# Optimization experiments

Measured on AMD Instinct MI355X. Metric: run time of the kernel, lower is better.

## Reference

```python
import jax, jax.numpy as jnp
import numpy as np

TEACHER_BOX = (-0.9, 0.9, -0.9, 0.9)  # x1, x2, y1, y2
STUDENT_BOX = (-0.8, 0.8, -0.8, 0.8)
STUDENT_TEMP = 0.1
TEACHER_TEMP = 0.04


def _box_grids(t_box, s_box, H, W):
    # Faithful to DINOLoss.box_to_grid: grid size derives from the TEACHER box,
    # meshgrid stacked as (y, x) -- torch quirk replicated (grid_sample reads ch0 as x).
    x1, x2, y1, y2 = t_box
    gW = int(abs(x1 - x2) / 2 * W)
    gH = int(abs(y1 - y2) / 2 * H)
    ty, tx = jnp.linspace(y1, y2, gH), jnp.linspace(x1, x2, gW)
    tgrid = jnp.stack(jnp.meshgrid(ty, tx, indexing='ij'), axis=-1)  # [gH, gW, 2]
    x1, x2, y1, y2 = s_box
    sy, sx = jnp.linspace(y1, y2, gH), jnp.linspace(x1, x2, gW)
    sgrid = jnp.stack(jnp.meshgrid(sy, sx, indexing='ij'), axis=-1)  # [gH, gW, 2]
    return tgrid, sgrid


def grid_sample_border(feat, grid):
    # feat: [B, C, H, W]; grid: [gh, gw, 2]; torch convention: grid[...,0]->x, grid[...,1]->y
    # bilinear, align_corners=False, padding_mode='border'
    B, C, H, W = feat.shape
    gx, gy = grid[..., 0], grid[..., 1]
    ix = jnp.clip(((gx + 1.0) * W - 1.0) * 0.5, 0.0, W - 1.0)
    iy = jnp.clip(((gy + 1.0) * H - 1.0) * 0.5, 0.0, H - 1.0)
    ix0 = jnp.floor(ix).astype(jnp.int32)
    iy0 = jnp.floor(iy).astype(jnp.int32)
    ix1 = jnp.clip(ix0 + 1, 0, W - 1)
    iy1 = jnp.clip(iy0 + 1, 0, H - 1)
    ix0 = jnp.clip(ix0, 0, W - 1)
    iy0 = jnp.clip(iy0, 0, H - 1)
    wx = ix - ix0
    wy = iy - iy0
    v00 = feat[:, :, iy0, ix0]  # [B, C, gh, gw]
    v01 = feat[:, :, iy0, ix1]
    v10 = feat[:, :, iy1, ix0]
    v11 = feat[:, :, iy1, ix1]
    return (v00 * (1 - wy) * (1 - wx) + v01 * (1 - wy) * wx
            + v10 * wy * (1 - wx) + v11 * wy * wx)


def setup_inputs() -> dict:
    key = jax.random.key(0)
    k1, k2, k3 = jax.random.split(key, 3)
    teacher_feat = jax.random.normal(k1, (8, 8192, 28, 28), dtype=jnp.float32)
    student_feat = jax.random.normal(k2, (8, 8192, 12, 12), dtype=jnp.float32)
    center = jax.random.normal(k3, (1, 8192), dtype=jnp.float32)
    return {"teacher_feat": teacher_feat, "student_feat": student_feat, "center": center}


def reference(teacher_feat, student_feat, center):
    H, W = teacher_feat.shape[-2:]
    tgrid, sgrid = _box_grids(TEACHER_BOX, STUDENT_BOX, H, W)
    # teacher: centered + sharpened softmax over channel dim (detached in original)
    t_prob = jax.nn.softmax((teacher_feat - center[:, :, None, None]) / TEACHER_TEMP, axis=1)
    t_common = jax.lax.stop_gradient(grid_sample_border(t_prob, tgrid))  # [B, C, gh, gw]
    s_common = grid_sample_border(student_feat / STUDENT_TEMP, sgrid)    # [B, C, gh, gw]
    loss = (-t_common * jax.nn.log_softmax(s_common, axis=1)).sum(axis=1).mean()
    return loss
```

## Files before the change

kernel.cpp:

```cpp
#include <hip/hip_runtime.h>
#include <hip/hip_bf16.h>

typedef __attribute__((ext_vector_type(8))) short  short8;
typedef __attribute__((ext_vector_type(4))) float  float4v;
typedef __attribute__((ext_vector_type(4))) unsigned short ushort4v;

#define NC    8192
#define TPIX  784
#define NB    8

#define WS_M2    0
#define WS_O     250880
#define WS_ZACC  283648
#define WS_DACC  308736
#define WS_ZPOS  333824
#define WS_ZERO_OFF WS_ZACC
#define WS_ZERO_LEN 70176
#define WS_STUDB 360448
#define WS_NEED  (360448 + 65536*320)

__device__ __forceinline__ unsigned short bf16rne(float f) {
    unsigned int u = __float_as_uint(f);
    u = (u + 0x7FFFu + ((u >> 16) & 1u)) >> 16;
    return (unsigned short)u;
}

__device__ __forceinline__ short8 cvt8(float4v a, float4v b) {
    union { __hip_bfloat162 h[4]; short8 s; } u;
    u.h[0] = __float22bfloat162_rn(float2{a[0], a[1]});
    u.h[1] = __float22bfloat162_rn(float2{a[2], a[3]});
    u.h[2] = __float22bfloat162_rn(float2{b[0], b[1]});
    u.h[3] = __float22bfloat162_rn(float2{b[2], b[3]});
    return u.s;
}

__global__ void k_init_m2(unsigned short* __restrict__ m2) {
    int p  = blockIdx.x;
    int sp = threadIdx.x;
    int y = p / 28, x = p % 28;
    float val = 0.f;
    if (sp < 144) {
        int v = sp / 12, u = sp % 12;
        float kyv = 0.f, kxu = 0.f;
        for (int a = 0; a < 25; ++a) {
            float ctc = 0.9f + 1.05f * (float)a;
            int   i0  = (int)ctc; float wt = ctc - (float)i0;
            float Ay  = (i0 == y) ? (1.f - wt) : ((i0 + 1 == y) ? wt : 0.f);
            float Ax  = (i0 == x) ? (1.f - wt) : ((i0 + 1 == x) ? wt : 0.f);
            float csc = 0.7f + 0.4f * (float)a;
            int   j0  = (int)csc; float wsv = csc - (float)j0;
            float Bv  = (j0 == v) ? (1.f - wsv) : ((j0 + 1 == v) ? wsv : 0.f);
            float Bu  = (j0 == u) ? (1.f - wsv) : ((j0 + 1 == u) ? wsv : 0.f);
            kyv += Ay * Bv;
            kxu += Ax * Bu;
        }
        val = 10.f * kyv * kxu;
    }
    m2[p * 160 + sp] = bf16rne(val);
}

__launch_bounds__(256)
__global__ void k_pre(const float* __restrict__ student, const float* __restrict__ center,
                      unsigned short* __restrict__ studb, float* __restrict__ o) {
    const int tid = blockIdx.x * 256 + threadIdx.x;
    const int row = tid / 20, ch = tid % 20;
    short8 hv = {0,0,0,0,0,0,0,0};
    if (ch < 18) {
        const float* src = student + (long long)row * 144 + ch * 8;
        hv = cvt8(*(const float4v*)(src), *(const float4v*)(src + 4));
    }
    *(short8*)(studb + (long long)row * 160 + ch * 8) = hv;
    if (ch == 0 && row < NC)
        o[row] = fmaf(36.0673762f, center[row], 233.7165966f);
}

template<bool PRE>
__launch_bounds__(256, 2)
__global__ void k_main(const float* __restrict__ teacher,
                       const float* __restrict__ student,
                       const float* __restrict__ center,
                       const unsigned short* __restrict__ m2,
                       const unsigned short* __restrict__ studb,
                       const float* __restrict__ o,
                       float* __restrict__ zacc, float* __restrict__ dacc) {
    const int b  = blockIdx.z;
    const int cg = blockIdx.y;
    const int t  = threadIdx.x;
    const int w = t >> 6, lane = t & 63, l15 = lane & 15, g = lane >> 4;

    const int tile0 = (blockIdx.x * 4 + w) * 2;
    const bool va = (tile0     < 49);
    const bool vb = (tile0 + 1 < 49);
    const int p0a = va ? tile0 * 16 : 0;
    const int p0b = vb ? (tile0 + 1) * 16 : 0;

    short8 afa[5], afb[5];
    {
        const unsigned short* ra = m2 + (p0a + l15) * 160;
        const unsigned short* rb = m2 + (p0b + l15) * 160;
        #pragma unroll
        for (int ks = 0; ks < 5; ++ks) {
            afa[ks] = *(const short8*)(ra + ks * 32 + g * 8);
            afb[ks] = *(const short8*)(rb + ks * 32 + g * 8);
        }
    }

    float sEa[4] = {0.f,0.f,0.f,0.f}, sEYa[4] = {0.f,0.f,0.f,0.f};
    float sEb[4] = {0.f,0.f,0.f,0.f}, sEYb[4] = {0.f,0.f,0.f,0.f};

    const long long tbase = (long long)(b * NC) * TPIX;
    const long long sbase = (long long)(b * NC) * 144;
    const short8 zfrag = {0,0,0,0,0,0,0,0};

    for (int cc = 0; cc < 8; ++cc) {
        const int cA = cg * 256 + cc * 32 + l15;
        const int cB = cA + 16;

        short8 bfA[5], bfB[5];
        float oA, oB;
        if (PRE) {
            const unsigned short* rA = studb + ((long long)(b * NC) + cA) * 160;
            const unsigned short* rB = rA + 16 * 160;
            #pragma unroll
            for (int ks = 0; ks < 5; ++ks) {
                bfA[ks] = *(const short8*)(rA + ks * 32 + g * 8);
                bfB[ks] = *(const short8*)(rB + ks * 32 + g * 8);
            }
            oA = o[cA];
            oB = o[cB];
        } else {
            const float* sA = student + sbase + (long long)cA * 144;
            const float* sB = sA + 16 * 144;
            #pragma unroll
            for (int ks = 0; ks < 4; ++ks) {
                bfA[ks] = cvt8(*(const float4v*)(sA + ks * 32 + g * 8),
                               *(const float4v*)(sA + ks * 32 + g * 8 + 4));
                bfB[ks] = cvt8(*(const float4v*)(sB + ks * 32 + g * 8),
                               *(const float4v*)(sB + ks * 32 + g * 8 + 4));
            }
            bfA[4] = (g < 2) ? cvt8(*(const float4v*)(sA + 128 + g * 8),
                                    *(const float4v*)(sA + 128 + g * 8 + 4)) : zfrag;
            bfB[4] = (g < 2) ? cvt8(*(const float4v*)(sB + 128 + g * 8),
                                    *(const float4v*)(sB + 128 + g * 8 + 4)) : zfrag;
            oA = fmaf(36.0673762f, center[cA], 233.7165966f);
            oB = fmaf(36.0673762f, center[cB], 233.7165966f);
        }

        const float* trA = teacher + tbase + (long long)cA * TPIX;
        const float* trB = trA + 16LL * TPIX;
        float4v tvAa = *(const float4v*)(trA + p0a + 4 * g);
        float4v tvAb = *(const float4v*)(trA + p0b + 4 * g);
        float4v tvBa = *(const float4v*)(trB + p0a + 4 * g);
        float4v tvBb = *(const float4v*)(trB + p0b + 4 * g);

        float4v accAa = {0.f,0.f,0.f,0.f}, accAb = {0.f,0.f,0.f,0.f};
        float4v accBa = {0.f,0.f,0.f,0.f}, accBb = {0.f,0.f,0.f,0.f};
        #pragma unroll
        for (int ks = 0; ks < 5; ++ks) {
            accAa = __builtin_amdgcn_mfma_f32_16x16x32_bf16(afa[ks], bfA[ks], accAa, 0, 0, 0);
            accAb = __builtin_amdgcn_mfma_f32_16x16x32_bf16(afb[ks], bfA[ks], accAb, 0, 0, 0);
            accBa = __builtin_amdgcn_mfma_f32_16x16x32_bf16(afa[ks], bfB[ks], accBa, 0, 0, 0);
            accBb = __builtin_amdgcn_mfma_f32_16x16x32_bf16(afb[ks], bfB[ks], accBb, 0, 0, 0);
        }

        #pragma unroll
        for (int i = 0; i < 4; ++i) {
            float e0 = exp2f(fmaf(36.0673762f, tvAa[i], -oA));
            sEa[i] += e0;  sEYa[i] = fmaf(e0, accAa[i], sEYa[i]);
            float e1 = exp2f(fmaf(36.0673762f, tvAb[i], -oA));
            sEb[i] += e1;  sEYb[i] = fmaf(e1, accAb[i], sEYb[i]);
            float e2 = exp2f(fmaf(36.0673762f, tvBa[i], -oB));
            sEa[i] += e2;  sEYa[i] = fmaf(e2, accBa[i], sEYa[i]);
            float e3 = exp2f(fmaf(36.0673762f, tvBb[i], -oB));
            sEb[i] += e3;  sEYb[i] = fmaf(e3, accBb[i], sEYb[i]);
        }
    }

    #pragma unroll
    for (int i = 0; i < 4; ++i) {
        float e0 = sEa[i], y0 = sEYa[i], e1 = sEb[i], y1 = sEYb[i];
        e0 += __shfl_xor(e0, 1); e0 += __shfl_xor(e0, 2); e0 += __shfl_xor(e0, 4); e0 += __shfl_xor(e0, 8);
        y0 += __shfl_xor(y0, 1); y0 += __shfl_xor(y0, 2); y0 += __shfl_xor(y0, 4); y0 += __shfl_xor(y0, 8);
        e1 += __shfl_xor(e1, 1); e1 += __shfl_xor(e1, 2); e1 += __shfl_xor(e1, 4); e1 += __shfl_xor(e1, 8);
        y1 += __shfl_xor(y1, 1); y1 += __shfl_xor(y1, 2); y1 += __shfl_xor(y1, 4); y1 += __shfl_xor(y1, 8);
        if (l15 == 0) {
            if (va) {
                atomicAdd(zacc + b * TPIX + p0a + 4 * g + i, e0);
                atomicAdd(dacc + b * TPIX + p0a + 4 * g + i, y0);
            }
            if (vb) {
                atomicAdd(zacc + b * TPIX + p0b + 4 * g + i, e1);
                atomicAdd(dacc + b * TPIX + p0b + 4 * g + i, y1);
            }
        }
    }
}

__launch_bounds__(256)
__global__ void k_lse(const float* __restrict__ student, float* __restrict__ zpos) {
    const int cg = blockIdx.x;
    const int a  = blockIdx.y;
    const int b  = blockIdx.z;
    const int t  = threadIdx.x;

    const float cv = 0.7f + 0.4f * (float)a;
    const int   v0 = (int)cv;
    const float wv = cv - (float)v0;
    const float W0 = 10.f * (1.f - wv), W1 = 10.f * wv;

    float accs[25];
    #pragma unroll
    for (int p = 0; p < 25; ++p) accs[p] = 0.f;

    for (int j = 0; j < 8; ++j) {
        const int c = cg * 2048 + 256 * j + t;
        const float* row = student + (long long)(b * NC + c) * 144 + v0 * 12;
        float4v r0 = *(const float4v*)(row + 0);
        float4v r1 = *(const float4v*)(row + 4);
        float4v r2 = *(const float4v*)(row + 8);
        float4v s0 = *(const float4v*)(row + 12);
        float4v s1 = *(const float4v*)(row + 16);
        float4v s2 = *(const float4v*)(row + 20);

        float R[12];
        #pragma unroll
        for (int u = 0; u < 4; ++u) {
            R[u]     = fmaf(W0, r0[u], W1 * s0[u]);
            R[u + 4] = fmaf(W0, r1[u], W1 * s1[u]);
            R[u + 8] = fmaf(W0, r2[u], W1 * s2[u]);
        }
        #pragma unroll
        for (int p = 0; p < 25; ++p) {
            const float cu = 0.7f + 0.4f * (float)p;
            const int   u0 = (int)cu;
            const float wu = cu - (float)u0;
            float sc = fmaf(1.f - wu, R[u0], wu * R[u0 + 1]);
            accs[p] += exp2f(fmaf(1.44269504f, sc, -86.5617025f));
        }
    }

    #pragma unroll
    for (int p = 0; p < 25; ++p) {
        float v = accs[p];
        #pragma unroll
        for (int m = 1; m < 64; m <<= 1) v += __shfl_xor(v, m);
        accs[p] = v;
    }
    if ((t & 63) == 0) {
        #pragma unroll
        for (int p = 0; p < 25; ++p)
            atomicAdd(zpos + (b * 25 + a) * 25 + p, accs[p]);
    }
}

__global__ void k_final(const float* __restrict__ zacc, const float* __restrict__ dacc,
                        const float* __restrict__ zpos, float* __restrict__ out) {
    __shared__ float red[8];
    int t = threadIdx.x;
    float s = 0.f;
    for (int i = t; i < 5000; i += 256) s += 60.f + logf(zpos[i]);
    for (int i = t; i < NB * TPIX; i += 256) s -= dacc[i] / zacc[i];
    for (int m = 1; m < 64; m <<= 1) s += __shfl_xor(s, m);
    if ((t & 63) == 0) red[t >> 6] = s;
    __syncthreads();
    if (t == 0) out[0] = (red[0] + red[1] + red[2] + red[3]) * (1.f / 5000.f);
}

extern "C" void kernel_launch(void* const* d_in, const int* in_sizes, int n_in,
                              void* d_out, int out_size, void* d_ws, size_t ws_size,
                              hipStream_t stream) {
    const float* teacher = (const float*)d_in[0];
    const float* student = (const float*)d_in[1];
    const float* center  = (const float*)d_in[2];

    char* ws = (char*)d_ws;
    unsigned short* m2    = (unsigned short*)(ws + WS_M2);
    float*          oarr  = (float*)(ws + WS_O);
    float*          zacc  = (float*)(ws + WS_ZACC);
    float*          dacc  = (float*)(ws + WS_DACC);
    float*          zpos  = (float*)(ws + WS_ZPOS);
    unsigned short* studb = (unsigned short*)(ws + WS_STUDB);

    hipMemsetAsync(ws + WS_ZERO_OFF, 0, WS_ZERO_LEN, stream);
    k_init_m2<<<784, 160, 0, stream>>>(m2);

    if (ws_size >= (size_t)WS_NEED) {
        k_pre<<<5120, 256, 0, stream>>>(student, center, studb, oarr);
        k_main<true><<<dim3(7, 32, 8), 256, 0, stream>>>(teacher, student, center, m2,
                                                         studb, oarr, zacc, dacc);
    } else {
        k_main<false><<<dim3(7, 32, 8), 256, 0, stream>>>(teacher, student, center, m2,
                                                          studb, oarr, zacc, dacc);
    }
    k_lse<<<dim3(4, 25, 8), 256, 0, stream>>>(student, zpos);
    k_final<<<1, 256, 0, stream>>>(zacc, dacc, zpos, (float*)d_out);
}
```

Measured before the change: 156.0 us.

## Stage interpolation matrix in LDS and tile six pixel tiles per wave

Adds a new main kernel that copies a 96-row slab of the bf16 interpolation matrix into shared memory. Each wave then walks its channels across six 16-pixel tiles, so every student fragment loaded from global memory is reused across six MFMA tiles instead of two. The grid shifts from many small blocks to 9x8x8 blocks of 512 threads, with 24 accumulator pairs per thread. This raises register pressure, adds LDS reads, and leaves some tiles idle in the last pixel group. The fallback kernel is simplified to process one channel group per iteration.

```diff
diff --git a/kernel.cpp b/kernel.cpp
--- a/kernel.cpp
+++ b/kernel.cpp
@@ -74,15 +74,93 @@
         o[row] = fmaf(36.0673762f, center[row], 233.7165966f);
 }
 
-template<bool PRE>
+__launch_bounds__(512, 4)
+__global__ void k_main2(const float* __restrict__ teacher,
+                        const unsigned short* __restrict__ m2,
+                        const unsigned short* __restrict__ studb,
+                        const float* __restrict__ o,
+                        float* __restrict__ zacc, float* __restrict__ dacc) {
+    __shared__ unsigned short m2s[96 * 168];
+
+    const int b  = blockIdx.z;
+    const int cw = blockIdx.y;
+    const int pg = blockIdx.x;
+    const int t  = threadIdx.x;
+    const int w = t >> 6, lane = t & 63, l15 = lane & 15, g = lane >> 4;
+
+    for (int i = t; i < 3840; i += 512) {
+        const int r = i / 40, c4 = i % 40;
+        const int rg = pg * 96 + r;
+        ushort4v v = {0, 0, 0, 0};
+        if (rg < TPIX) v = *(const ushort4v*)(m2 + rg * 160 + c4 * 4);
+        *(ushort4v*)&m2s[r * 168 + c4 * 4] = v;
+    }
+    __syncthreads();
+
+    float sE[24], sEY[24];
+    #pragma unroll
+    for (int j = 0; j < 24; ++j) { sE[j] = 0.f; sEY[j] = 0.f; }
+
+    const long long tbase = (long long)(b * NC) * TPIX;
+
+    for (int k = 0; k < 8; ++k) {
+        const int c = cw * 1024 + k * 128 + w * 16 + l15;
+
+        const unsigned short* srow = studb + ((long long)(b * NC) + c) * 160;
+        short8 bf[5];
+        #pragma unroll
+        for (int ks = 0; ks < 5; ++ks)
+            bf[ks] = *(const short8*)(srow + ks * 32 + g * 8);
+        const float oc = o[c];
+
+        const float* trow = teacher + tbase + (long long)c * TPIX;
+
+        #pragma unroll
+        for (int t6 = 0; t6 < 6; ++t6) {
+            if (pg * 6 + t6 > 48) continue;
+            const int p0 = pg * 96 + t6 * 16;
+
+            float4v tv = *(const float4v*)(trow + p0 + 4 * g);
+
+            float4v acc = {0.f, 0.f, 0.f, 0.f};
+            #pragma unroll
+            for (int ks = 0; ks < 5; ++ks) {
+                short8 af = *(const short8*)&m2s[(t6 * 16 + l15) * 168 + ks * 32 + g * 8];
+                acc = __builtin_amdgcn_mfma_f32_16x16x32_bf16(af, bf[ks], acc, 0, 0, 0);
+            }
+
+            #pragma unroll
+            for (int i = 0; i < 4; ++i) {
+                float e = exp2f(fmaf(36.0673762f, tv[i], -oc));
+                sE[t6 * 4 + i] += e;
+                sEY[t6 * 4 + i] = fmaf(e, acc[i], sEY[t6 * 4 + i]);
+            }
+        }
+    }
+
+    #pragma unroll
+    for (int t6 = 0; t6 < 6; ++t6) {
+        if (pg * 6 + t6 > 48) continue;
+        #pragma unroll
+        for (int i = 0; i < 4; ++i) {
+            float e = sE[t6 * 4 + i], y = sEY[t6 * 4 + i];
+            e += __shfl_xor(e, 1); e += __shfl_xor(e, 2); e += __shfl_xor(e, 4); e += __shfl_xor(e, 8);
+            y += __shfl_xor(y, 1); y += __shfl_xor(y, 2); y += __shfl_xor(y, 4); y += __shfl_xor(y, 8);
+            if (l15 == 0) {
+                const int p = pg * 96 + t6 * 16 + 4 * g + i;
+                atomicAdd(zacc + b * TPIX + p, e);
+                atomicAdd(dacc + b * TPIX + p, y);
+            }
+        }
+    }
+}
+
 __launch_bounds__(256, 2)
-__global__ void k_main(const float* __restrict__ teacher,
-                       const float* __restrict__ student,
-                       const float* __restrict__ center,
-                       const unsigned short* __restrict__ m2,
-                       const unsigned short* __restrict__ studb,
-                       const float* __restrict__ o,
-                       float* __restrict__ zacc, float* __restrict__ dacc) {
+__global__ void k_main_fb(const float* __restrict__ teacher,
+                          const float* __restrict__ student,
+                          const float* __restrict__ center,
+                          const unsigned short* __restrict__ m2,
+                          float* __restrict__ zacc, float* __restrict__ dacc) {
     const int b  = blockIdx.z;
     const int cg = blockIdx.y;
     const int t  = threadIdx.x;
@@ -107,72 +185,36 @@
 
     float sEa[4] = {0.f,0.f,0.f,0.f}, sEYa[4] = {0.f,0.f,0.f,0.f};
     float sEb[4] = {0.f,0.f,0.f,0.f}, sEYb[4] = {0.f,0.f,0.f,0.f};
-
     const long long tbase = (long long)(b * NC) * TPIX;
     const long long sbase = (long long)(b * NC) * 144;
     const short8 zfrag = {0,0,0,0,0,0,0,0};
 
-    for (int cc = 0; cc < 8; ++cc) {
-        const int cA = cg * 256 + cc * 32 + l15;
-        const int cB = cA + 16;
-
-        short8 bfA[5], bfB[5];
-        float oA, oB;
-        if (PRE) {
-            const unsigned short* rA = studb + ((long long)(b * NC) + cA) * 160;
-            const unsigned short* rB = rA + 16 * 160;
-            #pragma unroll
-            for (int ks = 0; ks < 5; ++ks) {
-                bfA[ks] = *(const short8*)(rA + ks * 32 + g * 8);
-                bfB[ks] = *(const short8*)(rB + ks * 32 + g * 8);
-            }
-            oA = o[cA];
-            oB = o[cB];
-        } else {
-            const float* sA = student + sbase + (long long)cA * 144;
-            const float* sB = sA + 16 * 144;
-            #pragma unroll
-            for (int ks = 0; ks < 4; ++ks) {
-                bfA[ks] = cvt8(*(const float4v*)(sA + ks * 32 + g * 8),
-                               *(const float4v*)(sA + ks * 32 + g * 8 + 4));
-                bfB[ks] = cvt8(*(const float4v*)(sB + ks * 32 + g * 8),
-                               *(const float4v*)(sB + ks * 32 + g * 8 + 4));
-            }
-            bfA[4] = (g < 2) ? cvt8(*(const float4v*)(sA + 128 + g * 8),
-                                    *(const float4v*)(sA + 128 + g * 8 + 4)) : zfrag;
-            bfB[4] = (g < 2) ? cvt8(*(const float4v*)(sB + 128 + g * 8),
-                                    *(const float4v*)(sB + 128 + g * 8 + 4)) : zfrag;
-            oA = fmaf(36.0673762f, center[cA], 233.7165966f);
-            oB = fmaf(36.0673762f, center[cB], 233.7165966f);
-        }
-
+    for (int cc = 0; cc < 16; ++cc) {
+        const int cA = cg * 256 + cc * 16 + l15;
+        const float* sA = student + sbase + (long long)cA * 144;
+        short8 bfA[5];
+        #pragma unroll
+        for (int ks = 0; ks < 4; ++ks)
+            bfA[ks] = cvt8(*(const float4v*)(sA + ks * 32 + g * 8),
+                           *(const float4v*)(sA + ks * 32 + g * 8 + 4));
+        bfA[4] = (g < 2) ? cvt8(*(const float4v*)(sA + 128 + g * 8),
+                                *(const float4v*)(sA + 128 + g * 8 + 4)) : zfrag;
+        const float oA = fmaf(36.0673762f, center[cA], 233.7165966f);
         const float* trA = teacher + tbase + (long long)cA * TPIX;
-        const float* trB = trA + 16LL * TPIX;
-        float4v tvAa = *(const float4v*)(trA + p0a + 4 * g);
-        float4v tvAb = *(const float4v*)(trA + p0b + 4 * g);
-        float4v tvBa = *(const float4v*)(trB + p0a + 4 * g);
-        float4v tvBb = *(const float4v*)(trB + p0b + 4 * g);
-
-        float4v accAa = {0.f,0.f,0.f,0.f}, accAb = {0.f,0.f,0.f,0.f};
-        float4v accBa = {0.f,0.f,0.f,0.f}, accBb = {0.f,0.f,0.f,0.f};
+        float4v tva = *(const float4v*)(trA + p0a + 4 * g);
+        float4v tvb = *(const float4v*)(trA + p0b + 4 * g);
+        float4v acca = {0.f,0.f,0.f,0.f}, accb = {0.f,0.f,0.f,0.f};
         #pragma unroll
         for (int ks = 0; ks < 5; ++ks) {
-            accAa = __builtin_amdgcn_mfma_f32_16x16x32_bf16(afa[ks], bfA[ks], accAa, 0, 0, 0);
-            accAb = __builtin_amdgcn_mfma_f32_16x16x32_bf16(afb[ks], bfA[ks], accAb, 0, 0, 0);
-            accBa = __builtin_amdgcn_mfma_f32_16x16x32_bf16(afa[ks], bfB[ks], accBa, 0, 0, 0);
-            accBb = __builtin_amdgcn_mfma_f32_16x16x32_bf16(afb[ks], bfB[ks], accBb, 0, 0, 0);
-        }
-
+            acca = __builtin_amdgcn_mfma_f32_16x16x32_bf16(afa[ks], bfA[ks], acca, 0, 0, 0);
+            accb = __builtin_amdgcn_mfma_f32_16x16x32_bf16(afb[ks], bfA[ks], accb, 0, 0, 0);
+        }
         #pragma unroll
         for (int i = 0; i < 4; ++i) {
-            float e0 = exp2f(fmaf(36.0673762f, tvAa[i], -oA));
-            sEa[i] += e0;  sEYa[i] = fmaf(e0, accAa[i], sEYa[i]);
-            float e1 = exp2f(fmaf(36.0673762f, tvAb[i], -oA));
-            sEb[i] += e1;  sEYb[i] = fmaf(e1, accAb[i], sEYb[i]);
-            float e2 = exp2f(fmaf(36.0673762f, tvBa[i], -oB));
-            sEa[i] += e2;  sEYa[i] = fmaf(e2, accBa[i], sEYa[i]);
-            float e3 = exp2f(fmaf(36.0673762f, tvBb[i], -oB));
-            sEb[i] += e3;  sEYb[i] = fmaf(e3, accBb[i], sEYb[i]);
+            float e0 = exp2f(fmaf(36.0673762f, tva[i], -oA));
+            sEa[i] += e0;  sEYa[i] = fmaf(e0, acca[i], sEYa[i]);
+            float e1 = exp2f(fmaf(36.0673762f, tvb[i], -oA));
+            sEb[i] += e1;  sEYb[i] = fmaf(e1, accb[i], sEYb[i]);
         }
     }
 
@@ -286,11 +328,9 @@
 
     if (ws_size >= (size_t)WS_NEED) {
         k_pre<<<5120, 256, 0, stream>>>(student, center, studb, oarr);
-        k_main<true><<<dim3(7, 32, 8), 256, 0, stream>>>(teacher, student, center, m2,
-                                                         studb, oarr, zacc, dacc);
+        k_main2<<<dim3(9, 8, 8), 512, 0, stream>>>(teacher, m2, studb, oarr, zacc, dacc);
     } else {
-        k_main<false><<<dim3(7, 32, 8), 256, 0, stream>>>(teacher, student, center, m2,
-                                                          studb, oarr, zacc, dacc);
+        k_main_fb<<<dim3(7, 32, 8), 256, 0, stream>>>(teacher, student, center, m2, zacc, dacc);
     }
     k_lse<<<dim3(4, 25, 8), 256, 0, stream>>>(student, zpos);
     k_final<<<1, 256, 0, stream>>>(zacc, dacc, zpos, (float*)d_out);
```

Measured after the change: 181.6 us. 16.4% more time.
